# Optimization experiments

Measured on AMD Instinct MI355X. Metric: run time of the kernel, lower is better.

Reference implementation:

```python
import jax, jax.numpy as jnp
import numpy as np


def setup_inputs() -> dict:
    key = jax.random.key(0)
    kq, kk, kv, ki, ks = jax.random.split(key, 5)
    B, H, S, D, VD, T = 2, 8, 2048, 64, 64, 128
    q = jax.random.normal(kq, (B, H, S, D), dtype=jnp.float32)
    k = jax.random.normal(kk, (B, H, S, D), dtype=jnp.float32)
    v = jax.random.normal(kv, (B, H, S, VD), dtype=jnp.float32)
    topk_indices = jax.random.randint(ki, (B, S, T), 0, S, dtype=jnp.int64)
    topk_scores = jax.random.uniform(ks, (B, S, T), dtype=jnp.float32)
    return {"q": q, "k": k, "v": v, "topk_indices": topk_indices,
            "topk_scores": topk_scores}


def reference(q, k, v, topk_indices, topk_scores):
    # q: (B,H,S,D), k: (B,H,S,D), v: (B,H,S,VD), topk_indices: (B,S,T)
    head_dim = q.shape[-1]
    scale = head_dim ** (-0.5)

    # Gather selected K/V per query directly (no O(S^2) expansion).
    # For each batch b: kb (H,S,D), idx (S,T) -> kb[:, idx, :] (H,S,T,D)
    gather = jax.vmap(lambda xb, ib: xb[:, ib, :])
    k_g = gather(k, topk_indices)  # (B,H,S,T,D)
    v_g = gather(v, topk_indices)  # (B,H,S,T,VD)

    # (B,H,S,T) scores
    attn_scores = jnp.einsum('bhsd,bhstd->bhst', q, k_g) * scale
    attn_weights = jax.nn.softmax(attn_scores, axis=-1)

    # reweight by indexer scores (broadcast over heads), then renormalize
    attn_weights = attn_weights * topk_scores[:, None, :, :]
    attn_weights = attn_weights / (attn_weights.sum(axis=-1, keepdims=True) + 1e-12)

    # (B,H,S,VD)
    output = jnp.einsum('bhst,bhstd->bhsd', attn_weights, v_g)
    return output
```

## Files before the change

### kernel.cpp

```cpp
#include <hip/hip_runtime.h>
#include <math.h>


#define BB 2
#define HH 8
#define SS 2048
#define DD 64
#define VDD 64
#define TT 128
#define SCALE 0.125f
#define LOG2E 1.44269504088896340736f
#define NKV (BB * HH * SS * DD)

typedef __fp16 h2 __attribute__((ext_vector_type(2)));
typedef float  f2 __attribute__((ext_vector_type(2)));

__device__ __forceinline__ float bf_lo(unsigned int u) {
    return __uint_as_float(u << 16);
}
__device__ __forceinline__ float bf_hi(unsigned int u) {
    return __uint_as_float(u);
}
__device__ __forceinline__ unsigned short f2bf_rne(float f) {
    unsigned int u = __float_as_uint(f);
    u += 0x7FFFu + ((u >> 16) & 1u);
    return (unsigned short)(u >> 16);
}
__device__ __forceinline__ unsigned int pk_f16(float x, float y) {
    h2 p = __builtin_amdgcn_cvt_pkrtz(x, y);
    return __builtin_bit_cast(unsigned int, p);
}
__device__ __forceinline__ float dot2(unsigned int qh, unsigned int kh, float c) {
    return __builtin_amdgcn_fdot2(__builtin_bit_cast(h2, qh),
                                  __builtin_bit_cast(h2, kh), c, false);
}

__global__ __launch_bounds__(256) void cvt_kv(
    const float* __restrict__ k, const float* __restrict__ v,
    unsigned int* __restrict__ kh, unsigned int* __restrict__ vb)
{
    int i = (blockIdx.x * 256 + threadIdx.x) * 4;
    if (i >= NKV) return;
    float4 kf = *(const float4*)(k + i);
    float4 vf = *(const float4*)(v + i);
    unsigned int k0 = pk_f16(kf.x, kf.y);
    unsigned int k1 = pk_f16(kf.z, kf.w);
    unsigned int v0 = (unsigned int)f2bf_rne(vf.x) | ((unsigned int)f2bf_rne(vf.y) << 16);
    unsigned int v1 = (unsigned int)f2bf_rne(vf.z) | ((unsigned int)f2bf_rne(vf.w) << 16);
    *(uint2*)(kh + i / 2) = make_uint2(k0, k1);
    *(uint2*)(vb + i / 2) = make_uint2(v0, v1);
}

__global__ __launch_bounds__(256, 4) void dsa_sparse_attn_bf16(
    const float* __restrict__ q,
    const unsigned int* __restrict__ kh,
    const unsigned int* __restrict__ vb,
    const int* __restrict__ topk_idx,
    const float* __restrict__ topk_sc,
    float* __restrict__ out)
{
    const int tid  = threadIdx.x;
    const int wave = tid >> 6;
    const int lane = tid & 63;
    const int h    = lane & 7;
    const int g    = lane >> 3;

    const int plane = blockIdx.x & 15;
    const int s     = (blockIdx.x >> 4) * 4 + wave;
    const int b     = plane >> 3;

    const float*        qp  = q  + ((size_t)plane * SS + s) * DD;
    const unsigned int* kp  = kh + (size_t)plane * SS * (DD / 2);
    const unsigned int* vp  = vb + (size_t)plane * SS * (VDD / 2);
    const int*          ip  = topk_idx + ((size_t)b * SS + s) * TT;
    const float*        scp = topk_sc  + ((size_t)b * SS + s) * TT;
    float*              op  = out + ((size_t)plane * SS + s) * VDD;

    int   iv0 = ip[lane];
    int   iv1 = ip[64 + lane];
    float sv0 = scp[lane];
    float sv1 = scp[64 + lane];
    float4 qa = *(const float4*)(qp + h * 8);
    float4 qb = *(const float4*)(qp + h * 8 + 4);
    const float QS = SCALE * LOG2E;
    unsigned int q0 = pk_f16(qa.x * QS, qa.y * QS);
    unsigned int q1 = pk_f16(qa.z * QS, qa.w * QS);
    unsigned int q2 = pk_f16(qb.x * QS, qb.y * QS);
    unsigned int q3 = pk_f16(qb.z * QS, qb.w * QS);

    f2 a0 = {0.f, 0.f}, a1 = {0.f, 0.f}, a2 = {0.f, 0.f}, a3 = {0.f, 0.f};
    float sum = 0.f;
    #pragma unroll
    for (int tc = 0; tc < 8; ++tc) {
        int   idx = __shfl(iv0, tc * 8 + g);
        float sc  = __shfl(sv0, tc * 8 + g);
        const size_t off = (size_t)idx * 32 + h * 4;
        uint4 kk = *(const uint4*)(kp + off);
        uint4 vv = *(const uint4*)(vp + off);
        float st = dot2(q0, kk.x, dot2(q1, kk.y, dot2(q2, kk.z, dot2(q3, kk.w, 0.f))));
        st += __shfl_xor(st, 1);
        st += __shfl_xor(st, 2);
        st += __shfl_xor(st, 4);
        float e = exp2f(st) * sc;
        sum += e;
        f2 ev = {e, e};
        f2 vx = {bf_lo(vv.x), bf_hi(vv.x)};
        f2 vy = {bf_lo(vv.y), bf_hi(vv.y)};
        f2 vz = {bf_lo(vv.z), bf_hi(vv.z)};
        f2 vw = {bf_lo(vv.w), bf_hi(vv.w)};
        a0 = __builtin_elementwise_fma(ev, vx, a0);
        a1 = __builtin_elementwise_fma(ev, vy, a1);
        a2 = __builtin_elementwise_fma(ev, vz, a2);
        a3 = __builtin_elementwise_fma(ev, vw, a3);
    }
    #pragma unroll
    for (int tc = 0; tc < 8; ++tc) {
        int   idx = __shfl(iv1, tc * 8 + g);
        float sc  = __shfl(sv1, tc * 8 + g);
        const size_t off = (size_t)idx * 32 + h * 4;
        uint4 kk = *(const uint4*)(kp + off);
        uint4 vv = *(const uint4*)(vp + off);
        float st = dot2(q0, kk.x, dot2(q1, kk.y, dot2(q2, kk.z, dot2(q3, kk.w, 0.f))));
        st += __shfl_xor(st, 1);
        st += __shfl_xor(st, 2);
        st += __shfl_xor(st, 4);
        float e = exp2f(st) * sc;
        sum += e;
        f2 ev = {e, e};
        f2 vx = {bf_lo(vv.x), bf_hi(vv.x)};
        f2 vy = {bf_lo(vv.y), bf_hi(vv.y)};
        f2 vz = {bf_lo(vv.z), bf_hi(vv.z)};
        f2 vw = {bf_lo(vv.w), bf_hi(vv.w)};
        a0 = __builtin_elementwise_fma(ev, vx, a0);
        a1 = __builtin_elementwise_fma(ev, vy, a1);
        a2 = __builtin_elementwise_fma(ev, vz, a2);
        a3 = __builtin_elementwise_fma(ev, vw, a3);
    }

    sum += __shfl_xor(sum, 8);
    sum += __shfl_xor(sum, 16);
    sum += __shfl_xor(sum, 32);

    float a[8] = {a0.x, a0.y, a1.x, a1.y, a2.x, a2.y, a3.x, a3.y};
    #pragma unroll
    for (int j = 0; j < 8; ++j) {
        a[j] += __shfl_xor(a[j], 8);
        a[j] += __shfl_xor(a[j], 16);
        a[j] += __shfl_xor(a[j], 32);
    }
    if (g == 0) {
        float inv = 1.0f / (sum + 1e-12f);
        *(float4*)(op + h * 8)     = make_float4(a[0] * inv, a[1] * inv, a[2] * inv, a[3] * inv);
        *(float4*)(op + h * 8 + 4) = make_float4(a[4] * inv, a[5] * inv, a[6] * inv, a[7] * inv);
    }
}

__global__ __launch_bounds__(256, 4) void dsa_sparse_attn_f32(
    const float* __restrict__ q,
    const float* __restrict__ k,
    const float* __restrict__ v,
    const int* __restrict__ topk_idx,
    const float* __restrict__ topk_sc,
    float* __restrict__ out)
{
    const int tid  = threadIdx.x;
    const int wave = tid >> 6;
    const int lane = tid & 63;
    const int plane = blockIdx.x & 15;
    const int s     = (blockIdx.x >> 4) * 4 + wave;
    const int b     = plane >> 3;

    const float* qp  = q + ((size_t)plane * SS + s) * DD;
    const float* kp  = k + (size_t)plane * SS * DD;
    const float* vp  = v + (size_t)plane * SS * VDD;
    const int*   ip  = topk_idx + ((size_t)b * SS + s) * TT;
    const float* scp = topk_sc  + ((size_t)b * SS + s) * TT;
    float*       op  = out + ((size_t)plane * SS + s) * VDD;

    __shared__ int   s_idx[4][TT];
    __shared__ float s_w[4][TT];

    float sc0 = scp[lane];
    float sc1 = scp[64 + lane];
    s_idx[wave][lane]      = ip[lane];
    s_idx[wave][64 + lane] = ip[64 + lane];

    const int l = lane & 3;
    const int g = lane >> 2;
    float4 qf[4];
    #pragma unroll
    for (int j = 0; j < 4; ++j) qf[j] = *(const float4*)(qp + l * 4 + 16 * j);
    __syncthreads();

    #pragma unroll
    for (int tc = 0; tc < 8; ++tc) {
        int t = tc * 16 + g;
        const float* krow = kp + (size_t)s_idx[wave][t] * DD;
        float acc = 0.f;
        #pragma unroll
        for (int j = 0; j < 4; ++j) {
            float4 kf = *(const float4*)(krow + l * 4 + 16 * j);
            acc += qf[j].x * kf.x + qf[j].y * kf.y + qf[j].z * kf.z + qf[j].w * kf.w;
        }
        acc += __shfl_xor(acc, 1);
        acc += __shfl_xor(acc, 2);
        if (l == 0) s_w[wave][t] = acc * SCALE;
    }
    __syncthreads();

    float a0 = s_w[wave][lane];
    float a1 = s_w[wave][64 + lane];
    float m = fmaxf(a0, a1);
    #pragma unroll
    for (int off = 32; off >= 1; off >>= 1) m = fmaxf(m, __shfl_xor(m, off));
    float e0 = __expf(a0 - m) * sc0;
    float e1 = __expf(a1 - m) * sc1;
    float sum = e0 + e1;
    #pragma unroll
    for (int off = 32; off >= 1; off >>= 1) sum += __shfl_xor(sum, off);
    float inv = 1.0f / (sum + 1e-12f);
    s_w[wave][lane]      = e0 * inv;
    s_w[wave][64 + lane] = e1 * inv;
    __syncthreads();

    float acc = 0.f;
    #pragma unroll 8
    for (int t = 0; t < TT; ++t)
        acc = fmaf(s_w[wave][t], vp[(size_t)s_idx[wave][t] * VDD + lane], acc);
    op[lane] = acc;
}

extern "C" void kernel_launch(void* const* d_in, const int* in_sizes, int n_in,
                              void* d_out, int out_size, void* d_ws, size_t ws_size,
                              hipStream_t stream) {
    const float* q   = (const float*)d_in[0];
    const float* k   = (const float*)d_in[1];
    const float* v   = (const float*)d_in[2];
    const int*   idx = (const int*)d_in[3];
    const float* sc  = (const float*)d_in[4];
    float*       out = (float*)d_out;

    const size_t need = (size_t)NKV * 2 * 2;
    if (ws_size >= need) {
        unsigned int* kh = (unsigned int*)d_ws;
        unsigned int* vb = kh + NKV / 2;
        hipLaunchKernelGGL(cvt_kv, dim3(NKV / 4 / 256), dim3(256), 0, stream,
                           k, v, kh, vb);
        hipLaunchKernelGGL(dsa_sparse_attn_bf16, dim3(8192), dim3(256), 0, stream,
                           q, kh, vb, idx, sc, out);
    } else {
        hipLaunchKernelGGL(dsa_sparse_attn_f32, dim3(8192), dim3(256), 0, stream,
                           q, k, v, idx, sc, out);
    }
}
```

Before: 124.6 us.

## Interleave K/V rows into one buffer and use DPP reductions with fast exp/rcp

```diff
diff --git a/kernel.cpp b/kernel.cpp
--- a/kernel.cpp
+++ b/kernel.cpp
@@ -35,9 +35,35 @@
                                   __builtin_bit_cast(h2, kh), c, false);
 }
 
+template <int CTRL>
+__device__ __forceinline__ float dpp_add(float x) {
+    int t = __builtin_amdgcn_update_dpp(0, __builtin_bit_cast(int, x),
+                                        CTRL, 0xF, 0xF, true);
+    return x + __builtin_bit_cast(float, t);
+}
+#define DPP_XOR1 0xB1
+#define DPP_XOR2 0x4E
+#define DPP_OQUAD 0x141
+#define DPP_XOR8 0x128
+
+__device__ __forceinline__ float fast_exp2(float x) {
+#if __has_builtin(__builtin_amdgcn_exp2f)
+    return __builtin_amdgcn_exp2f(x);
+#else
+    return exp2f(x);
+#endif
+}
+__device__ __forceinline__ float fast_rcp(float x) {
+#if __has_builtin(__builtin_amdgcn_rcpf)
+    return __builtin_amdgcn_rcpf(x);
+#else
+    return 1.0f / x;
+#endif
+}
+
 __global__ __launch_bounds__(256) void cvt_kv(
     const float* __restrict__ k, const float* __restrict__ v,
-    unsigned int* __restrict__ kh, unsigned int* __restrict__ vb)
+    unsigned int* __restrict__ kv)
 {
     int i = (blockIdx.x * 256 + threadIdx.x) * 4;
     if (i >= NKV) return;
@@ -47,14 +73,16 @@
     unsigned int k1 = pk_f16(kf.z, kf.w);
     unsigned int v0 = (unsigned int)f2bf_rne(vf.x) | ((unsigned int)f2bf_rne(vf.y) << 16);
     unsigned int v1 = (unsigned int)f2bf_rne(vf.z) | ((unsigned int)f2bf_rne(vf.w) << 16);
-    *(uint2*)(kh + i / 2) = make_uint2(k0, k1);
-    *(uint2*)(vb + i / 2) = make_uint2(v0, v1);
+    int r = i >> 6;
+    int c = (i & 63) >> 1;
+    unsigned int* row = kv + (size_t)r * 64;
+    *(uint2*)(row + c)      = make_uint2(k0, k1);
+    *(uint2*)(row + 32 + c) = make_uint2(v0, v1);
 }
 
 __global__ __launch_bounds__(256, 4) void dsa_sparse_attn_bf16(
     const float* __restrict__ q,
-    const unsigned int* __restrict__ kh,
-    const unsigned int* __restrict__ vb,
+    const unsigned int* __restrict__ kv,
     const int* __restrict__ topk_idx,
     const float* __restrict__ topk_sc,
     float* __restrict__ out)
@@ -64,17 +92,18 @@
     const int lane = tid & 63;
     const int h    = lane & 7;
     const int g    = lane >> 3;
+    const int g4   = g << 2;
+    const int h16  = h << 4;
 
     const int plane = blockIdx.x & 15;
     const int s     = (blockIdx.x >> 4) * 4 + wave;
     const int b     = plane >> 3;
 
-    const float*        qp  = q  + ((size_t)plane * SS + s) * DD;
-    const unsigned int* kp  = kh + (size_t)plane * SS * (DD / 2);
-    const unsigned int* vp  = vb + (size_t)plane * SS * (VDD / 2);
-    const int*          ip  = topk_idx + ((size_t)b * SS + s) * TT;
-    const float*        scp = topk_sc  + ((size_t)b * SS + s) * TT;
-    float*              op  = out + ((size_t)plane * SS + s) * VDD;
+    const float* qp  = q  + ((size_t)plane * SS + s) * DD;
+    const char*  kvp = (const char*)(kv + (size_t)plane * (SS * 64));
+    const int*   ip  = topk_idx + ((size_t)b * SS + s) * TT;
+    const float* scp = topk_sc  + ((size_t)b * SS + s) * TT;
+    float*       op  = out + ((size_t)plane * SS + s) * VDD;
 
     int   iv0 = ip[lane];
     int   iv1 = ip[64 + lane];
@@ -91,17 +120,27 @@
     f2 a0 = {0.f, 0.f}, a1 = {0.f, 0.f}, a2 = {0.f, 0.f}, a3 = {0.f, 0.f};
     float sum = 0.f;
     #pragma unroll
-    for (int tc = 0; tc < 8; ++tc) {
-        int   idx = __shfl(iv0, tc * 8 + g);
-        float sc  = __shfl(sv0, tc * 8 + g);
-        const size_t off = (size_t)idx * 32 + h * 4;
-        uint4 kk = *(const uint4*)(kp + off);
-        uint4 vv = *(const uint4*)(vp + off);
+    for (int tc = 0; tc < 16; ++tc) {
+        const int sel = g4 + (tc & 7) * 32;
+        int   idx;
+        float sc;
+        if (tc < 8) {
+            idx = __builtin_amdgcn_ds_bpermute(sel, iv0);
+            sc  = __builtin_bit_cast(float,
+                  __builtin_amdgcn_ds_bpermute(sel, __builtin_bit_cast(int, sv0)));
+        } else {
+            idx = __builtin_amdgcn_ds_bpermute(sel, iv1);
+            sc  = __builtin_bit_cast(float,
+                  __builtin_amdgcn_ds_bpermute(sel, __builtin_bit_cast(int, sv1)));
+        }
+        const unsigned int voff = ((unsigned int)idx << 8) + h16;
+        uint4 kk = *(const uint4*)(kvp + voff);
+        uint4 vv = *(const uint4*)(kvp + voff + 128);
         float st = dot2(q0, kk.x, dot2(q1, kk.y, dot2(q2, kk.z, dot2(q3, kk.w, 0.f))));
-        st += __shfl_xor(st, 1);
-        st += __shfl_xor(st, 2);
-        st += __shfl_xor(st, 4);
-        float e = exp2f(st) * sc;
+        st = dpp_add<DPP_XOR1>(st);
+        st = dpp_add<DPP_XOR2>(st);
+        st = dpp_add<DPP_OQUAD>(st);
+        float e = fast_exp2(st) * sc;
         sum += e;
         f2 ev = {e, e};
         f2 vx = {bf_lo(vv.x), bf_hi(vv.x)};
@@ -113,43 +152,20 @@
         a2 = __builtin_elementwise_fma(ev, vz, a2);
         a3 = __builtin_elementwise_fma(ev, vw, a3);
     }
-    #pragma unroll
-    for (int tc = 0; tc < 8; ++tc) {
-        int   idx = __shfl(iv1, tc * 8 + g);
-        float sc  = __shfl(sv1, tc * 8 + g);
-        const size_t off = (size_t)idx * 32 + h * 4;
-        uint4 kk = *(const uint4*)(kp + off);
-        uint4 vv = *(const uint4*)(vp + off);
-        float st = dot2(q0, kk.x, dot2(q1, kk.y, dot2(q2, kk.z, dot2(q3, kk.w, 0.f))));
-        st += __shfl_xor(st, 1);
-        st += __shfl_xor(st, 2);
-        st += __shfl_xor(st, 4);
-        float e = exp2f(st) * sc;
-        sum += e;
-        f2 ev = {e, e};
-        f2 vx = {bf_lo(vv.x), bf_hi(vv.x)};
-        f2 vy = {bf_lo(vv.y), bf_hi(vv.y)};
-        f2 vz = {bf_lo(vv.z), bf_hi(vv.z)};
-        f2 vw = {bf_lo(vv.w), bf_hi(vv.w)};
-        a0 = __builtin_elementwise_fma(ev, vx, a0);
-        a1 = __builtin_elementwise_fma(ev, vy, a1);
-        a2 = __builtin_elementwise_fma(ev, vz, a2);
-        a3 = __builtin_elementwise_fma(ev, vw, a3);
-    }
-
-    sum += __shfl_xor(sum, 8);
+
+    sum = dpp_add<DPP_XOR8>(sum);
     sum += __shfl_xor(sum, 16);
     sum += __shfl_xor(sum, 32);
 
     float a[8] = {a0.x, a0.y, a1.x, a1.y, a2.x, a2.y, a3.x, a3.y};
     #pragma unroll
     for (int j = 0; j < 8; ++j) {
-        a[j] += __shfl_xor(a[j], 8);
+        a[j] = dpp_add<DPP_XOR8>(a[j]);
         a[j] += __shfl_xor(a[j], 16);
         a[j] += __shfl_xor(a[j], 32);
     }
     if (g == 0) {
-        float inv = 1.0f / (sum + 1e-12f);
+        float inv = fast_rcp(sum + 1e-12f);
         *(float4*)(op + h * 8)     = make_float4(a[0] * inv, a[1] * inv, a[2] * inv, a[3] * inv);
         *(float4*)(op + h * 8 + 4) = make_float4(a[4] * inv, a[5] * inv, a[6] * inv, a[7] * inv);
     }
@@ -242,12 +258,11 @@
 
     const size_t need = (size_t)NKV * 2 * 2;
     if (ws_size >= need) {
-        unsigned int* kh = (unsigned int*)d_ws;
-        unsigned int* vb = kh + NKV / 2;
+        unsigned int* kv = (unsigned int*)d_ws;
         hipLaunchKernelGGL(cvt_kv, dim3(NKV / 4 / 256), dim3(256), 0, stream,
-                           k, v, kh, vb);
+                           k, v, kv);
         hipLaunchKernelGGL(dsa_sparse_attn_bf16, dim3(8192), dim3(256), 0, stream,
-                           q, kh, vb, idx, sc, out);
+                           q, kv, idx, sc, out);
     } else {
         hipLaunchKernelGGL(dsa_sparse_attn_f32, dim3(8192), dim3(256), 0, stream,
                            q, k, v, idx, sc, out);
```

Measured after the change: 117.5 us, median of 2. -5.7%, faster.
